# Optimization experiments

Measured on AMD Instinct MI355X. Metric: run time of the kernel, lower is better.

Reference implementation:

```python
import jax, jax.numpy as jnp
import numpy as np

TAU = 0.5
EPS = 1e-8


def setup_inputs() -> dict:
    key = jax.random.key(0)
    k1, k2 = jax.random.split(key)
    N, D = 200000, 512
    z_pos = jax.random.normal(k1, (N, D), dtype=jnp.float32)
    W = jax.random.normal(k2, (D, D), dtype=jnp.float32) * (1.0 / np.sqrt(D))
    b = jnp.zeros((D,), dtype=jnp.float32)
    return {"z_pos": z_pos, "W": W, "b": b}


def reference(z_pos, W, b):
    # sample_centroid: softmax-weighted centroid (computed on detached embeddings)
    h = jax.lax.stop_gradient(z_pos)
    init_c = h.mean(axis=0)                              # [D]
    d2 = jnp.sum((h - init_c[None, :]) ** 2, axis=1)     # [N]
    w = jax.nn.softmax(-d2 / TAU)                        # [N]
    c = jnp.sum(h * w[:, None], axis=0)                  # [D]

    # SimNet: dist = 1 - cosine_similarity(proj(x), c)
    x_proj = z_pos @ W.T + b                             # [N, D]
    x_norm = jnp.maximum(jnp.linalg.norm(x_proj, axis=-1), EPS)  # [N]
    c_norm = jnp.maximum(jnp.linalg.norm(c), EPS)
    cos = (x_proj @ c) / (x_norm * c_norm)               # [N]
    dist = 1.0 - cos
    return dist
```

## Files before the change

### kernel.cpp

```cpp
#include <hip/hip_runtime.h>
#include <hip/hip_bf16.h>
#include <math.h>

#define DD 512
#define EPSF 1e-8f
#define BM 128
#define BN 128
#define BK 32
#define FBIG 3.402823466e+38f
#define NPART 2048

typedef __bf16 bf16_t;
typedef __bf16 bf16x4_t __attribute__((ext_vector_type(4)));
typedef __bf16 bf16x8_t __attribute__((ext_vector_type(8)));
typedef float f32x4 __attribute__((ext_vector_type(4)));

__device__ inline float bf2f(unsigned short u) {
    return __uint_as_float(((unsigned int)u) << 16);
}

__global__ void k_convW(const float* __restrict__ W, bf16_t* __restrict__ Wb) {
    int i = blockIdx.x * blockDim.x + threadIdx.x;
    float4 v = ((const float4*)W)[i];
    bf16x4_t o;
    o[0] = (bf16_t)v.x; o[1] = (bf16_t)v.y; o[2] = (bf16_t)v.z; o[3] = (bf16_t)v.w;
    ((bf16x4_t*)Wb)[i] = o;
}

template<bool CONV>
__global__ void k_colsum(const float* __restrict__ z, bf16_t* __restrict__ zb,
                         float* __restrict__ part, int N, int rpb) {
    int t = threadIdx.x;
    int b = blockIdx.x;
    int col4 = t & 127, sub = t >> 7;
    int r0 = b * rpb, r1 = min(r0 + rpb, N);
    const float4* z4 = (const float4*)z;
    float4 acc = make_float4(0.f, 0.f, 0.f, 0.f);
    #pragma unroll 4
    for (int r = r0 + sub; r < r1; r += 2) {
        float4 v = z4[(size_t)r * 128 + col4];
        if (CONV) {
            bf16x4_t o;
            o[0] = (bf16_t)v.x; o[1] = (bf16_t)v.y; o[2] = (bf16_t)v.z; o[3] = (bf16_t)v.w;
            ((bf16x4_t*)zb)[(size_t)r * 128 + col4] = o;
        }
        acc.x += v.x; acc.y += v.y; acc.z += v.z; acc.w += v.w;
    }
    __shared__ float4 sm[128];
    if (sub == 1) sm[col4] = acc;
    __syncthreads();
    if (sub == 0) {
        float4 o = sm[col4];
        acc.x += o.x; acc.y += o.y; acc.z += o.z; acc.w += o.w;
        ((float4*)(part + (size_t)b * DD))[col4] = acc;
    }
}

__global__ void k_reduceP(const float* __restrict__ part, float* __restrict__ outv, float scale) {
    __shared__ float sm[256];
    int j = blockIdx.x;
    int t = threadIdx.x;
    float s = 0.f;
    #pragma unroll
    for (int p = 0; p < NPART / 256; ++p) s += part[(size_t)(p * 256 + t) * DD + j];
    sm[t] = s;
    __syncthreads();
    for (int st = 128; st > 0; st >>= 1) {
        if (t < st) sm[t] += sm[t + st];
        __syncthreads();
    }
    if (t == 0) outv[j] = sm[0] * scale;
}

__global__ __launch_bounds__(256, 4) void k_d2w(
    const float* __restrict__ z, const float* __restrict__ cbar,
    float* __restrict__ part, float* __restrict__ mpart,
    float* __restrict__ spart, int N)
{
    __shared__ float4 cs[128];
    __shared__ float4 vsm[4][128];
    __shared__ float wm[4], wsv[4];
    int t = threadIdx.x;
    int lane = t & 63, wv = t >> 6;
    int l15 = lane & 15, r4 = lane >> 4;
    if (t < 128) cs[t] = ((const float4*)cbar)[t];
    __syncthreads();

    int gw = (blockIdx.x * 256 + t) >> 6;
    int nw = (gridDim.x * 256) >> 6;
    float m = FBIG, s = 0.f;
    float4 acc[8];
    #pragma unroll
    for (int q = 0; q < 8; ++q) acc[q] = make_float4(0.f, 0.f, 0.f, 0.f);

    for (int r = gw * 4 + r4; r < N; r += nw * 4) {
        const float4* zr = (const float4*)(z + (size_t)r * DD);
        float4 vv[8];
        float sum = 0.f;
        #pragma unroll
        for (int q = 0; q < 8; ++q) {
            float4 v = zr[q * 16 + l15];
            float4 c = cs[q * 16 + l15];
            vv[q] = v;
            float d;
            d = v.x - c.x; sum += d * d;
            d = v.y - c.y; sum += d * d;
            d = v.z - c.z; sum += d * d;
            d = v.w - c.w; sum += d * d;
        }
        #pragma unroll
        for (int off = 1; off < 16; off <<= 1) sum += __shfl_xor(sum, off, 64);
        float w;
        if (sum < m) {
            float f = __expf(-2.0f * (m - sum));
            s *= f;
            #pragma unroll
            for (int q = 0; q < 8; ++q) {
                acc[q].x *= f; acc[q].y *= f; acc[q].z *= f; acc[q].w *= f;
            }
            m = sum;
            w = 1.0f;
        } else {
            w = __expf(-2.0f * (sum - m));
        }
        s += w;
        #pragma unroll
        for (int q = 0; q < 8; ++q) {
            acc[q].x += w * vv[q].x; acc[q].y += w * vv[q].y;
            acc[q].z += w * vv[q].z; acc[q].w += w * vv[q].w;
        }
    }

    float mw = fminf(m, __shfl_xor(m, 16, 64));
    mw = fminf(mw, __shfl_xor(mw, 32, 64));
    float f = __expf(-2.0f * (m - mw));
    s *= f;
    #pragma unroll
    for (int q = 0; q < 8; ++q) {
        acc[q].x *= f; acc[q].y *= f; acc[q].z *= f; acc[q].w *= f;
    }
    #pragma unroll
    for (int off = 16; off < 64; off <<= 1) {
        s += __shfl_xor(s, off, 64);
        #pragma unroll
        for (int q = 0; q < 8; ++q) {
            acc[q].x += __shfl_xor(acc[q].x, off, 64);
            acc[q].y += __shfl_xor(acc[q].y, off, 64);
            acc[q].z += __shfl_xor(acc[q].z, off, 64);
            acc[q].w += __shfl_xor(acc[q].w, off, 64);
        }
    }
    if (lane < 16) {
        #pragma unroll
        for (int q = 0; q < 8; ++q) vsm[wv][q * 16 + l15] = acc[q];
        if (lane == 0) { wm[wv] = mw; wsv[wv] = s; }
    }
    __syncthreads();
    if (t < 128) {
        float M = fminf(fminf(wm[0], wm[1]), fminf(wm[2], wm[3]));
        float4 o = make_float4(0.f, 0.f, 0.f, 0.f);
        #pragma unroll
        for (int w2 = 0; w2 < 4; ++w2) {
            float fw = __expf(-2.0f * (wm[w2] - M));
            float4 a = vsm[w2][t];
            o.x += fw * a.x; o.y += fw * a.y; o.z += fw * a.z; o.w += fw * a.w;
        }
        ((float4*)(part + (size_t)blockIdx.x * DD))[t] = o;
        if (t == 0) {
            float S = 0.f;
            #pragma unroll
            for (int w2 = 0; w2 < 4; ++w2) S += wsv[w2] * __expf(-2.0f * (wm[w2] - M));
            mpart[blockIdx.x] = M;
            spart[blockIdx.x] = S;
        }
    }
}

__global__ void k_combine2(const float* __restrict__ mpart, const float* __restrict__ spart,
                           float* __restrict__ wscale) {
    __shared__ float smm[256], sms[256];
    int t = threadIdx.x;
    float M = FBIG;
    for (int i = t; i < NPART; i += 256) M = fminf(M, mpart[i]);
    smm[t] = M;
    __syncthreads();
    for (int st = 128; st > 0; st >>= 1) {
        if (t < st) smm[t] = fminf(smm[t], smm[t + st]);
        __syncthreads();
    }
    M = smm[0];
    float S = 0.f;
    for (int i = t; i < NPART; i += 256) S += spart[i] * __expf(-2.0f * (mpart[i] - M));
    sms[t] = S;
    __syncthreads();
    for (int st = 128; st > 0; st >>= 1) {
        if (t < st) sms[t] += sms[t + st];
        __syncthreads();
    }
    float inv = 1.0f / sms[0];
    for (int i = t; i < NPART; i += 256) wscale[i] = __expf(-2.0f * (mpart[i] - M)) * inv;
}

__global__ void k_reducePW(const float* __restrict__ part, const float* __restrict__ wscale,
                           float* __restrict__ outv) {
    __shared__ float sm[256];
    int j = blockIdx.x, t = threadIdx.x;
    float s = 0.f;
    #pragma unroll
    for (int p = 0; p < NPART / 256; ++p) {
        int b = p * 256 + t;
        s += part[(size_t)b * DD + j] * wscale[b];
    }
    sm[t] = s;
    __syncthreads();
    for (int st = 128; st > 0; st >>= 1) {
        if (t < st) sm[t] += sm[t + st];
        __syncthreads();
    }
    if (t == 0) outv[j] = sm[0];
}

__global__ void k_cnorm(const float* __restrict__ cvec, float* __restrict__ outp) {
    __shared__ float sm[512];
    float v = cvec[threadIdx.x];
    sm[threadIdx.x] = v * v;
    __syncthreads();
    for (int st = 256; st > 0; st >>= 1) {
        if (threadIdx.x < st) sm[threadIdx.x] += sm[threadIdx.x + st];
        __syncthreads();
    }
    if (threadIdx.x == 0) outp[0] = 1.0f / fmaxf(sqrtf(sm[0]), EPSF);
}

__global__ __launch_bounds__(512, 2) void k_gemm256(
    const bf16_t* __restrict__ zb, const bf16_t* __restrict__ Wb,
    const float* __restrict__ bvec, const float* __restrict__ cvec,
    float* __restrict__ sqp, float* __restrict__ dtp, int N, int npad)
{
    __shared__ bf16_t As[2 * 2 * 128 * 64];
    __shared__ bf16_t Bs[2 * 2 * 128 * 64];

    const int t    = threadIdx.x;
    const int lane = t & 63;
    const int wid  = t >> 6;
    const int wr   = wid >> 2;
    const int wc   = wid & 3;
    const int quad = lane >> 4;
    const int l15  = lane & 15;

    const int nwg = gridDim.x * gridDim.y;
    const int lid = blockIdx.y * gridDim.x + blockIdx.x;
    const int q8  = nwg >> 3, r8 = nwg & 7;
    const int xcd = lid & 7, idx = lid >> 3;
    const int wg  = (xcd < r8 ? xcd * (q8 + 1) : r8 * (q8 + 1) + (xcd - r8) * q8) + idx;
    const int cb     = wg & 1;
    const int row0   = (wg >> 1) * 256;

    const int tr = t >> 3;
    const int bo = ((t & 7) * 16) ^ ((tr & 7) << 4);
    const char* apt = (const char*)zb + (size_t)(row0 + tr) * (DD * 2) + bo;
    const char* bpt = (const char*)Wb + (size_t)(cb * 256 + tr) * (DD * 2) + bo;
    const int ldsw = __builtin_amdgcn_readfirstlane(wid * 1024);

#define STAGEALL(buf, kt) do {                                                              \
    _Pragma("unroll")                                                                       \
    for (int h_ = 0; h_ < 2; ++h_) {                                                        \
        _Pragma("unroll")                                                                   \
        for (int j_ = 0; j_ < 2; ++j_) {                                                    \
            __builtin_amdgcn_global_load_lds(                                               \
                (const __attribute__((address_space(1))) unsigned int*)(const void*)        \
                    (apt + (size_t)(h_ * 128 + j_ * 64) * 1024 + (kt) * 128),               \
                (__attribute__((address_space(3))) unsigned int*)(void*)                    \
                    ((char*)As + (buf) * 32768 + h_ * 16384 + j_ * 8192 + ldsw), 16, 0, 0); \
            __builtin_amdgcn_global_load_lds(                                               \
                (const __attribute__((address_space(1))) unsigned int*)(const void*)        \
                    (bpt + (size_t)(h_ * 128 + j_ * 64) * 1024 + (kt) * 128),               \
                (__attribute__((address_space(3))) unsigned int*)(void*)                    \
                    ((char*)Bs + (buf) * 32768 + h_ * 16384 + j_ * 8192 + ldsw), 16, 0, 0); \
        }                                                                                   \
    }                                                                                       \
} while (0)

    const char* abase = (const char*)As + wr * 16384 + l15 * 128;
    const char* bbase = (const char*)Bs + (wc >> 1) * 16384 + ((wc & 1) * 64 + l15) * 128;
    const int kq = quad * 16;
    const int sw = (l15 & 7) << 4;

    f32x4 acc[8][4];
    #pragma unroll
    for (int m = 0; m < 8; ++m)
        #pragma unroll
        for (int n = 0; n < 4; ++n) acc[m][n] = (f32x4){0.f, 0.f, 0.f, 0.f};

    STAGEALL(0, 0);
    asm volatile("s_waitcnt vmcnt(0)" ::: "memory");
    __builtin_amdgcn_sched_barrier(0);
    __builtin_amdgcn_s_barrier();
    __builtin_amdgcn_sched_barrier(0);

    #pragma unroll
    for (int kt = 0; kt < 8; ++kt) {
        const int cur = kt & 1;
        if (kt < 7) STAGEALL(cur ^ 1, kt + 1);
        __builtin_amdgcn_sched_barrier(0);
        __builtin_amdgcn_s_setprio(1);
        #pragma unroll
        for (int s = 0; s < 2; ++s) {
            const int kb = (s * 64 + kq) ^ sw;
            bf16x8_t afr[8], bfr[4];
            #pragma unroll
            for (int m = 0; m < 8; ++m)
                afr[m] = *(const bf16x8_t*)(abase + cur * 32768 + m * 2048 + kb);
            #pragma unroll
            for (int n = 0; n < 4; ++n)
                bfr[n] = *(const bf16x8_t*)(bbase + cur * 32768 + n * 2048 + kb);
            #pragma unroll
            for (int m = 0; m < 8; ++m)
                #pragma unroll
                for (int n = 0; n < 4; ++n)
                    acc[m][n] = __builtin_amdgcn_mfma_f32_16x16x32_bf16(
                        afr[m], bfr[n], acc[m][n], 0, 0, 0);
        }
        __builtin_amdgcn_s_setprio(0);
        if (kt < 7) { asm volatile("s_waitcnt vmcnt(0)" ::: "memory"); }
        __builtin_amdgcn_sched_barrier(0);
        __builtin_amdgcn_s_barrier();
        __builtin_amdgcn_sched_barrier(0);
    }
#undef STAGEALL

    float* psq = (float*)As;
    float* pdt = (float*)((char*)As + 16384);
    float bc[4], cc[4];
    #pragma unroll
    for (int n = 0; n < 4; ++n) {
        int col = cb * 256 + wc * 64 + n * 16 + l15;
        bc[n] = bvec[col];
        cc[n] = cvec[col];
    }
    #pragma unroll
    for (int m = 0; m < 8; ++m) {
        #pragma unroll
        for (int rg = 0; rg < 4; ++rg) {
            float sq = 0.f, dt = 0.f;
            #pragma unroll
            for (int n = 0; n < 4; ++n) {
                float x = acc[m][n][rg] + bc[n];
                sq += x * x;
                dt += x * cc[n];
            }
            sq += __shfl_xor(sq, 1, 64); dt += __shfl_xor(dt, 1, 64);
            sq += __shfl_xor(sq, 2, 64); dt += __shfl_xor(dt, 2, 64);
            if ((l15 & 3) == 0) {
                int row = wr * 128 + m * 16 + quad * 4 + rg;
                int slot = wc * 4 + (l15 >> 2);
                psq[row * 16 + slot] = sq;
                pdt[row * 16 + slot] = dt;
            }
        }
    }
    __syncthreads();
    if (t < 256) {
        int r = row0 + t;
        if (r < N) {
            const float4* p4 = (const float4*)(psq + t * 16);
            const float4* d4 = (const float4*)(pdt + t * 16);
            float sq = 0.f, dt = 0.f;
            #pragma unroll
            for (int i = 0; i < 4; ++i) {
                float4 a = p4[i], b2 = d4[i];
                sq += a.x + a.y + a.z + a.w;
                dt += b2.x + b2.y + b2.z + b2.w;
            }
            sqp[(size_t)cb * npad + r] = sq;
            dtp[(size_t)cb * npad + r] = dt;
        }
    }
}

__global__ __launch_bounds__(256, 4) void k_gemm_fb(
    const float* __restrict__ z, const bf16_t* __restrict__ Wb,
    const float* __restrict__ bvec, const float* __restrict__ cvec,
    float* __restrict__ sqp, float* __restrict__ dtp, int N, int npad)
{
    __shared__ bf16_t Asl[BM * BK];
    __shared__ bf16_t Bsl[BN * BK];
    __shared__ float psq[BM][8];
    __shared__ float pdt[BM][8];

    const int t    = threadIdx.x;
    const int lane = t & 63;
    const int wv   = t >> 6;
    const int wrr  = wv >> 1;
    const int wcc  = wv & 1;
    const int quad = lane >> 4;
    const int l15  = lane & 15;
    const int cbx  = blockIdx.x;
    const int row0 = blockIdx.y * BM;

    const bf16_t* bp = Wb + (size_t)(cbx * BN + (t >> 2)) * DD + (t & 3) * 8;
    const int arow = t >> 1;
    const int ah   = t & 1;
    int rowe = row0 + arow; if (rowe >= N) rowe = N - 1;
    const float4* zp4 = (const float4*)(z + (size_t)rowe * DD + ah * 16);

    f32x4 acc[4][4];
    #pragma unroll
    for (int a = 0; a < 4; ++a)
        #pragma unroll
        for (int b = 0; b < 4; ++b) acc[a][b] = (f32x4){0.f, 0.f, 0.f, 0.f};

    float4 v0 = zp4[0], v1 = zp4[1], v2 = zp4[2], v3 = zp4[3];

    for (int kc = 0; kc < DD; kc += BK) {
        if (kc) __syncthreads();
        #pragma unroll
        for (int q = 0; q < 2; ++q) {
            int ldsoff = __builtin_amdgcn_readfirstlane(q * 4096 + wv * 1024);
            __builtin_amdgcn_global_load_lds(
                (const __attribute__((address_space(1))) unsigned int*)(const void*)(bp + (size_t)q * 64 * DD + kc),
                (__attribute__((address_space(3))) unsigned int*)(void*)((char*)Bsl + ldsoff),
                16, 0, 0);
        }
        bf16x8_t lo, hi;
        lo[0]=(bf16_t)v0.x; lo[1]=(bf16_t)v0.y; lo[2]=(bf16_t)v0.z; lo[3]=(bf16_t)v0.w;
        lo[4]=(bf16_t)v1.x; lo[5]=(bf16_t)v1.y; lo[6]=(bf16_t)v1.z; lo[7]=(bf16_t)v1.w;
        hi[0]=(bf16_t)v2.x; hi[1]=(bf16_t)v2.y; hi[2]=(bf16_t)v2.z; hi[3]=(bf16_t)v2.w;
        hi[4]=(bf16_t)v3.x; hi[5]=(bf16_t)v3.y; hi[6]=(bf16_t)v3.z; hi[7]=(bf16_t)v3.w;
        *(bf16x8_t*)(Asl + arow * BK + ah * 16)     = lo;
        *(bf16x8_t*)(Asl + arow * BK + ah * 16 + 8) = hi;
        __syncthreads();
        if (kc + BK < DD) {
            int kf = (kc + BK) >> 2;
            v0 = zp4[kf]; v1 = zp4[kf + 1]; v2 = zp4[kf + 2]; v3 = zp4[kf + 3];
        }
        bf16x8_t af[4];
        #pragma unroll
        for (int rt = 0; rt < 4; ++rt)
            af[rt] = *(const bf16x8_t*)(Asl + (wrr * 64 + rt * 16 + l15) * BK + quad * 8);
        #pragma unroll
        for (int ct = 0; ct < 4; ++ct) {
            bf16x8_t bfv = *(const bf16x8_t*)(Bsl + (wcc * 64 + ct * 16 + l15) * BK + quad * 8);
            #pragma unroll
            for (int rt = 0; rt < 4; ++rt)
                acc[rt][ct] = __builtin_amdgcn_mfma_f32_16x16x32_bf16(af[rt], bfv, acc[rt][ct], 0, 0, 0);
        }
    }

    float bc[4], cc[4];
    #pragma unroll
    for (int ct = 0; ct < 4; ++ct) {
        int col = cbx * BN + wcc * 64 + ct * 16 + l15;
        bc[ct] = bvec[col];
        cc[ct] = cvec[col];
    }
    #pragma unroll
    for (int rt = 0; rt < 4; ++rt) {
        #pragma unroll
        for (int rg = 0; rg < 4; ++rg) {
            float sq = 0.f, dt = 0.f;
            #pragma unroll
            for (int ct = 0; ct < 4; ++ct) {
                float x = acc[rt][ct][rg] + bc[ct];
                sq += x * x;
                dt += x * cc[ct];
            }
            sq += __shfl_xor(sq, 1, 64); dt += __shfl_xor(dt, 1, 64);
            sq += __shfl_xor(sq, 2, 64); dt += __shfl_xor(dt, 2, 64);
            if ((l15 & 3) == 0) {
                int rl = wrr * 64 + rt * 16 + quad * 4 + rg;
                psq[rl][wcc * 4 + (l15 >> 2)] = sq;
                pdt[rl][wcc * 4 + (l15 >> 2)] = dt;
            }
        }
    }
    __syncthreads();
    if (t < BM) {
        int r = row0 + t;
        if (r < N) {
            float sq = 0.f, dt = 0.f;
            #pragma unroll
            for (int i = 0; i < 8; ++i) { sq += psq[t][i]; dt += pdt[t][i]; }
            sqp[(size_t)cbx * npad + r] = sq;
            dtp[(size_t)cbx * npad + r] = dt;
        }
    }
}

template<int NCB>
__global__ void k_final(const float* __restrict__ sqp, const float* __restrict__ dtp,
                        const float* __restrict__ cninv, float* __restrict__ out,
                        int N, int npad) {
    int r = blockIdx.x * blockDim.x + threadIdx.x;
    if (r < N) {
        float sq = 0.f, dt = 0.f;
        #pragma unroll
        for (int i = 0; i < NCB; ++i) {
            sq += sqp[(size_t)i * npad + r];
            dt += dtp[(size_t)i * npad + r];
        }
        out[r] = 1.0f - dt * cninv[0] / fmaxf(sqrtf(sq), EPSF);
    }
}

extern "C" void kernel_launch(void* const* d_in, const int* in_sizes, int n_in,
                              void* d_out, int out_size, void* d_ws, size_t ws_size,
                              hipStream_t stream)
{
    const float* z = (const float*)d_in[0];
    const float* W = (const float*)d_in[1];
    const float* b = (const float*)d_in[2];
    float* out = (float*)d_out;
    int N = in_sizes[0] / DD;
    int npad = ((N + 255) / 256) * 256;

    float* ws = (float*)d_ws;
    size_t off = 0;
    float* part   = ws + off; off += (size_t)NPART * DD;
    float* cbar   = ws + off; off += DD;
    float* mpart  = ws + off; off += NPART;
    float* spart  = ws + off; off += NPART;
    float* wscale = ws + off; off += NPART;
    float* cvec   = ws + off; off += DD;
    float* cninv  = ws + off; off += 1;
    off = (off + 3) & ~(size_t)3;
    float* sqp    = ws + off; off += (size_t)4 * npad;
    float* dtp    = ws + off; off += (size_t)4 * npad;
    bf16_t* Wb    = (bf16_t*)(ws + off); off += (size_t)DD * DD / 2;
    bf16_t* zb    = (bf16_t*)(ws + off);
    size_t need_bytes = (off + (size_t)npad * DD / 2) * sizeof(float);
    const bool use_zb = ws_size >= need_bytes;

    int rpb = (N + NPART - 1) / NPART;

    k_convW<<<256, 256, 0, stream>>>(W, Wb);
    if (use_zb) k_colsum<true ><<<NPART, 256, 0, stream>>>(z, zb, part, N, rpb);
    else        k_colsum<false><<<NPART, 256, 0, stream>>>(z, zb, part, N, rpb);
    k_reduceP<<<DD, 256, 0, stream>>>(part, cbar, 1.0f / (float)N);
    k_d2w<<<NPART, 256, 0, stream>>>(z, cbar, part, mpart, spart, N);
    k_combine2<<<1, 256, 0, stream>>>(mpart, spart, wscale);
    k_reducePW<<<DD, 256, 0, stream>>>(part, wscale, cvec);
    k_cnorm<<<1, DD, 0, stream>>>(cvec, cninv);
    if (use_zb) {
        dim3 grid(2, npad / 256);
        k_gemm256<<<grid, 512, 0, stream>>>(zb, Wb, b, cvec, sqp, dtp, N, npad);
        k_final<2><<<(N + 255) / 256, 256, 0, stream>>>(sqp, dtp, cninv, out, N, npad);
    } else {
        dim3 grid(4, npad / BM);
        k_gemm_fb<<<grid, 256, 0, stream>>>(z, Wb, b, cvec, sqp, dtp, N, npad);
        k_final<4><<<(N + 255) / 256, 256, 0, stream>>>(sqp, dtp, cninv, out, N, npad);
    }
}
```

Baseline: 878.9 us.

## Shrink GEMM tile to 128x256 and read W fragments directly from global

```diff
diff --git a/kernel.cpp b/kernel.cpp
--- a/kernel.cpp
+++ b/kernel.cpp
@@ -232,19 +232,18 @@
     if (threadIdx.x == 0) outp[0] = 1.0f / fmaxf(sqrtf(sm[0]), EPSF);
 }
 
-__global__ __launch_bounds__(512, 2) void k_gemm256(
+__global__ __launch_bounds__(512, 4) void k_gemm256(
     const bf16_t* __restrict__ zb, const bf16_t* __restrict__ Wb,
     const float* __restrict__ bvec, const float* __restrict__ cvec,
     float* __restrict__ sqp, float* __restrict__ dtp, int N, int npad)
 {
-    __shared__ bf16_t As[2 * 2 * 128 * 64];
-    __shared__ bf16_t Bs[2 * 2 * 128 * 64];
+    __shared__ bf16_t As[2 * 128 * 64];
 
     const int t    = threadIdx.x;
     const int lane = t & 63;
     const int wid  = t >> 6;
-    const int wr   = wid >> 2;
-    const int wc   = wid & 3;
+    const int wm   = wid >> 2;
+    const int wn   = wid & 3;
     const int quad = lane >> 4;
     const int l15  = lane & 15;
 
@@ -253,46 +252,37 @@
     const int q8  = nwg >> 3, r8 = nwg & 7;
     const int xcd = lid & 7, idx = lid >> 3;
     const int wg  = (xcd < r8 ? xcd * (q8 + 1) : r8 * (q8 + 1) + (xcd - r8) * q8) + idx;
-    const int cb     = wg & 1;
-    const int row0   = (wg >> 1) * 256;
+    const int cb   = wg & 1;
+    const int row0 = (wg >> 1) * 128;
 
     const int tr = t >> 3;
     const int bo = ((t & 7) * 16) ^ ((tr & 7) << 4);
-    const char* apt = (const char*)zb + (size_t)(row0 + tr) * (DD * 2) + bo;
-    const char* bpt = (const char*)Wb + (size_t)(cb * 256 + tr) * (DD * 2) + bo;
+    const char* apt = (const char*)zb + (size_t)(row0 + tr) * 1024 + bo;
     const int ldsw = __builtin_amdgcn_readfirstlane(wid * 1024);
 
-#define STAGEALL(buf, kt) do {                                                              \
+#define STAGE_A(buf, kt) do {                                                               \
     _Pragma("unroll")                                                                       \
-    for (int h_ = 0; h_ < 2; ++h_) {                                                        \
-        _Pragma("unroll")                                                                   \
-        for (int j_ = 0; j_ < 2; ++j_) {                                                    \
-            __builtin_amdgcn_global_load_lds(                                               \
-                (const __attribute__((address_space(1))) unsigned int*)(const void*)        \
-                    (apt + (size_t)(h_ * 128 + j_ * 64) * 1024 + (kt) * 128),               \
-                (__attribute__((address_space(3))) unsigned int*)(void*)                    \
-                    ((char*)As + (buf) * 32768 + h_ * 16384 + j_ * 8192 + ldsw), 16, 0, 0); \
-            __builtin_amdgcn_global_load_lds(                                               \
-                (const __attribute__((address_space(1))) unsigned int*)(const void*)        \
-                    (bpt + (size_t)(h_ * 128 + j_ * 64) * 1024 + (kt) * 128),               \
-                (__attribute__((address_space(3))) unsigned int*)(void*)                    \
-                    ((char*)Bs + (buf) * 32768 + h_ * 16384 + j_ * 8192 + ldsw), 16, 0, 0); \
-        }                                                                                   \
+    for (int r_ = 0; r_ < 2; ++r_) {                                                        \
+        __builtin_amdgcn_global_load_lds(                                                   \
+            (const __attribute__((address_space(1))) unsigned int*)(const void*)            \
+                (apt + (size_t)r_ * 65536 + (kt) * 128),                                    \
+            (__attribute__((address_space(3))) unsigned int*)(void*)                        \
+                ((char*)As + (buf) * 16384 + r_ * 8192 + ldsw), 16, 0, 0);                  \
     }                                                                                       \
 } while (0)
 
-    const char* abase = (const char*)As + wr * 16384 + l15 * 128;
-    const char* bbase = (const char*)Bs + (wc >> 1) * 16384 + ((wc & 1) * 64 + l15) * 128;
+    const char* abase = (const char*)As + (wm * 64 + l15) * 128;
     const int kq = quad * 16;
     const int sw = (l15 & 7) << 4;
-
-    f32x4 acc[8][4];
-    #pragma unroll
-    for (int m = 0; m < 8; ++m)
+    const bf16_t* bptr = Wb + (size_t)(cb * 256 + wn * 64 + l15) * DD + quad * 8;
+
+    f32x4 acc[4][4];
+    #pragma unroll
+    for (int m = 0; m < 4; ++m)
         #pragma unroll
         for (int n = 0; n < 4; ++n) acc[m][n] = (f32x4){0.f, 0.f, 0.f, 0.f};
 
-    STAGEALL(0, 0);
+    STAGE_A(0, 0);
     asm volatile("s_waitcnt vmcnt(0)" ::: "memory");
     __builtin_amdgcn_sched_barrier(0);
     __builtin_amdgcn_s_barrier();
@@ -301,45 +291,45 @@
     #pragma unroll
     for (int kt = 0; kt < 8; ++kt) {
         const int cur = kt & 1;
-        if (kt < 7) STAGEALL(cur ^ 1, kt + 1);
+        if (kt < 7) STAGE_A(cur ^ 1, kt + 1);
         __builtin_amdgcn_sched_barrier(0);
         __builtin_amdgcn_s_setprio(1);
         #pragma unroll
         for (int s = 0; s < 2; ++s) {
             const int kb = (s * 64 + kq) ^ sw;
-            bf16x8_t afr[8], bfr[4];
-            #pragma unroll
-            for (int m = 0; m < 8; ++m)
-                afr[m] = *(const bf16x8_t*)(abase + cur * 32768 + m * 2048 + kb);
+            bf16x8_t bfr[4], afr[4];
             #pragma unroll
             for (int n = 0; n < 4; ++n)
-                bfr[n] = *(const bf16x8_t*)(bbase + cur * 32768 + n * 2048 + kb);
-            #pragma unroll
-            for (int m = 0; m < 8; ++m)
+                bfr[n] = *(const bf16x8_t*)(bptr + n * (16 * DD) + kt * 64 + s * 32);
+            #pragma unroll
+            for (int m = 0; m < 4; ++m)
+                afr[m] = *(const bf16x8_t*)(abase + cur * 16384 + m * 2048 + kb);
+            #pragma unroll
+            for (int m = 0; m < 4; ++m)
                 #pragma unroll
                 for (int n = 0; n < 4; ++n)
                     acc[m][n] = __builtin_amdgcn_mfma_f32_16x16x32_bf16(
                         afr[m], bfr[n], acc[m][n], 0, 0, 0);
         }
         __builtin_amdgcn_s_setprio(0);
-        if (kt < 7) { asm volatile("s_waitcnt vmcnt(0)" ::: "memory"); }
+        asm volatile("s_waitcnt vmcnt(0)" ::: "memory");
         __builtin_amdgcn_sched_barrier(0);
         __builtin_amdgcn_s_barrier();
         __builtin_amdgcn_sched_barrier(0);
     }
-#undef STAGEALL
+#undef STAGE_A
 
     float* psq = (float*)As;
-    float* pdt = (float*)((char*)As + 16384);
+    float* pdt = (float*)As + 2048;
     float bc[4], cc[4];
     #pragma unroll
     for (int n = 0; n < 4; ++n) {
-        int col = cb * 256 + wc * 64 + n * 16 + l15;
+        int col = cb * 256 + wn * 64 + n * 16 + l15;
         bc[n] = bvec[col];
         cc[n] = cvec[col];
     }
     #pragma unroll
-    for (int m = 0; m < 8; ++m) {
+    for (int m = 0; m < 4; ++m) {
         #pragma unroll
         for (int rg = 0; rg < 4; ++rg) {
             float sq = 0.f, dt = 0.f;
@@ -352,15 +342,15 @@
             sq += __shfl_xor(sq, 1, 64); dt += __shfl_xor(dt, 1, 64);
             sq += __shfl_xor(sq, 2, 64); dt += __shfl_xor(dt, 2, 64);
             if ((l15 & 3) == 0) {
-                int row = wr * 128 + m * 16 + quad * 4 + rg;
-                int slot = wc * 4 + (l15 >> 2);
+                int row = wm * 64 + m * 16 + quad * 4 + rg;
+                int slot = wn * 4 + (l15 >> 2);
                 psq[row * 16 + slot] = sq;
                 pdt[row * 16 + slot] = dt;
             }
         }
     }
     __syncthreads();
-    if (t < 256) {
+    if (t < 128) {
         int r = row0 + t;
         if (r < N) {
             const float4* p4 = (const float4*)(psq + t * 16);
@@ -512,7 +502,7 @@
     const float* b = (const float*)d_in[2];
     float* out = (float*)d_out;
     int N = in_sizes[0] / DD;
-    int npad = ((N + 255) / 256) * 256;
+    int npad = ((N + 127) / 128) * 128;
 
     float* ws = (float*)d_ws;
     size_t off = 0;
@@ -542,7 +532,7 @@
     k_reducePW<<<DD, 256, 0, stream>>>(part, wscale, cvec);
     k_cnorm<<<1, DD, 0, stream>>>(cvec, cninv);
     if (use_zb) {
-        dim3 grid(2, npad / 256);
+        dim3 grid(2, npad / 128);
         k_gemm256<<<grid, 512, 0, stream>>>(zb, Wb, b, cvec, sqp, dtp, N, npad);
         k_final<2><<<(N + 255) / 256, 256, 0, stream>>>(sqp, dtp, cninv, out, N, npad);
     } else {
```

Measured after the change: 939.7 us. 6.9% more time.
